# Kernel optimization log

Measured on AMD Instinct MI355X. Metric: run time of the kernel, lower is better.

The kernel has to match this reference:

```python
import jax, jax.numpy as jnp
import numpy as np

# ---- st-moe constants (training-mode routing) ----
EPS = 1e-9
TOP_N = 2
CAP_FACTOR = 1.25      # capacity_factor_train
THRESHOLD = 0.2        # threshold_train (2nd expert)
BAL_COEF = 0.01
Z_COEF = 0.001
MIN_CAP = 4
LN_EPS = 1e-5

B, N, D, E = 4, 2048, 512, 8
H = int(D * 4 * 2 / 3)  # 1365, st-moe default Expert hidden


def _rms_norm(x, gamma):
    # F.normalize(x, dim=-1) * sqrt(d) * gamma
    nrm = jnp.maximum(jnp.linalg.norm(x, axis=-1, keepdims=True), 1e-12)
    return x / nrm * (x.shape[-1] ** 0.5) * gamma


def setup_inputs() -> dict:
    key = jax.random.key(0)
    ks = jax.random.split(key, 6)
    s = 0.02
    return {
        "x": jax.random.normal(ks[0], (B, N, D), jnp.float32),
        "gate_w": jax.random.normal(ks[1], (D, E), jnp.float32) * s,
        "prenorm_g": jnp.ones((D,), jnp.float32),
        "w1": jax.random.normal(ks[2], (E, D, 2 * H), jnp.float32) * s,
        "b1": jnp.zeros((E, 2 * H), jnp.float32),
        "mult_bias": jnp.ones((E, H), jnp.float32),
        "w2": jax.random.normal(ks[3], (E, H, D), jnp.float32) * s,
        "b2": jnp.zeros((E, D), jnp.float32),
        "ln_g": jnp.ones((D,), jnp.float32),
        "ln_b": jnp.zeros((D,), jnp.float32),
    }


def _stmoe_fnn(x, gate_w, prenorm_g, w1, b1, mult_bias, w2, b2, ln_g, ln_b):
    b, n, d = x.shape
    e = gate_w.shape[1]
    cap = max(MIN_CAP, min(n, int(n * CAP_FACTOR / e)))  # static python int

    # SparseMoEBlock: moe(RMSNorm(x)) + x
    xg = _rms_norm(x, prenorm_g)

    # ---- TopNGating ----
    gate_logits = jnp.einsum('bnd,de->bne', xg, gate_w)
    raw_gates = jax.nn.softmax(gate_logits, axis=-1)
    gates, idx = jax.lax.top_k(raw_gates, TOP_N)          # (b,n,k)
    gates = jnp.moveaxis(gates, -1, 0)                    # (k,b,n)
    idx = jnp.moveaxis(idx, -1, 0)                        # (k,b,n)
    one_hot = jax.nn.one_hot(idx, e, dtype=x.dtype)       # (k,b,n,e)

    denom = jnp.maximum(gates.sum(axis=0), EPS)
    gates = gates / denom                                 # normalized top-n scores

    # stochastic routing to non-first experts: prob = min(1, gate/threshold)
    thresh = jnp.array([EPS, THRESHOLD], x.dtype)[:, None, None]
    probs = jax.random.uniform(jax.random.key(42), gates.shape, x.dtype)
    should_route = probs < (gates / jnp.maximum(thresh, EPS))
    should_route = should_route.at[0].set(True)
    mask = one_hot * should_route[..., None].astype(x.dtype)  # (k,b,n,e)

    # exclusive cumsum over sequence -> position within each expert
    mask_cumsum = jnp.cumsum(mask, axis=-2) - mask

    positions, kept_masks = [], []
    prev_count = jnp.zeros((b, 1, e), x.dtype)
    for k in range(TOP_N):  # top_n=2, tiny static loop
        pos_in_expert = (mask_cumsum[k] + prev_count) * mask[k]      # (b,n,e)
        kept = mask[k] * (pos_in_expert < float(cap)).astype(x.dtype)
        prev_count = prev_count + kept.sum(axis=-2, keepdims=True)
        positions.append(pos_in_expert.sum(axis=-1))                 # (b,n)
        kept_masks.append(kept)
    mask = jnp.stack(kept_masks)       # (k,b,n,e) post-capacity
    positions = jnp.stack(positions)   # (k,b,n)

    mask_flat = mask.sum(axis=-1)      # (k,b,n)
    gates = gates * mask_flat

    # safe one-hot: out-of-range (overflow) positions map to all-zeros
    pos_one_hot = jax.nn.one_hot(positions.astype(jnp.int32), cap, dtype=x.dtype)  # (k,b,n,c)
    combine = jnp.einsum('kbn,kbne,kbnc->bnec', gates, one_hot, pos_one_hot)       # (b,n,e,c)

    # straight-through dispatch tensor
    dispatch = (combine > 0).astype(x.dtype) + combine - jax.lax.stop_gradient(combine)

    # ---- dispatch, expert GEGLU FFN, combine ----
    expert_in = jnp.einsum('bnd,bnec->becd', xg, dispatch)                 # (b,e,c,d)
    h = jnp.einsum('becd,edf->becf', expert_in, w1) + b1[None, :, None, :]
    u, g = jnp.split(h, 2, axis=-1)
    act = u * jax.nn.gelu(g, approximate=False) * mult_bias[None, :, None, :]
    expert_out = jnp.einsum('bech,ehd->becd', act, w2) + b2[None, :, None, :]
    moe_out = jnp.einsum('becd,bnec->bnd', expert_out, combine)

    # ---- aux losses (training mode) ----
    density_1 = mask[0].mean(axis=-2)          # (b,e), post-capacity mask (torch in-place view)
    density_proxy = raw_gates.mean(axis=-2)    # (b,e)
    balance_loss = (density_proxy * density_1).mean() * float(e ** 2)
    z = jax.nn.logsumexp(gate_logits, axis=-1)
    router_z_loss = jnp.mean(z * z)
    total_aux = BAL_COEF * balance_loss + Z_COEF * router_z_loss

    # residual, (dropout -> identity for determinism), LayerNorm
    y = moe_out + x
    mu = y.mean(axis=-1, keepdims=True)
    var = jnp.mean((y - mu) ** 2, axis=-1, keepdims=True)
    out = (y - mu) * jax.lax.rsqrt(var + LN_EPS) * ln_g + ln_b
    return out, total_aux


def reference(x, gate_w, prenorm_g, w1, b1, mult_bias, w2, b2, ln_g, ln_b):
    return _stmoe_fnn(x, gate_w, prenorm_g, w1, b1, mult_bias, w2, b2, ln_g, ln_b)
```

## Files before the change

### kernel.cpp

```cpp
#include <hip/hip_runtime.h>
#include <hip/hip_bf16.h>
#include <math.h>

#define BB 4
#define NN 2048
#define DD 512
#define EE 8
#define HH 1365
#define H2 2730
#define CAP 320
#define NT (BB*NN)
#define KP2 1408
#define NW1 2816
#define ME 1280

typedef __bf16 bf16_t;
typedef __bf16 bf16x8 __attribute__((ext_vector_type(8)));
typedef float f32x4 __attribute__((ext_vector_type(4)));

__device__ __forceinline__ float gelu_exact(float x){
    return 0.5f * x * (1.0f + erff(x * 0.70710678118654752f));
}
__device__ __forceinline__ void gl2lds16(const void* g, void* s){
    __builtin_amdgcn_global_load_lds((const __attribute__((address_space(1))) unsigned int*)g,
                                     (__attribute__((address_space(3))) unsigned int*)s,
                                     16, 0, 0);
}
__device__ __forceinline__ unsigned rotl32(unsigned x, int d){ return (x<<d)|(x>>(32-d)); }
__device__ __forceinline__ void tf_round(unsigned &x0, unsigned &x1, int r){
    x0 += x1; x1 = rotl32(x1, r); x1 ^= x0;
}
__device__ float threefry_u01_second(unsigned t){
    const unsigned ks0 = 0u, ks1 = 42u, ks2 = 0x1BD11BDAu ^ 42u;
    unsigned x0 = t, x1 = t + 8192u;
    x0 += ks0; x1 += ks1;
    tf_round(x0,x1,13); tf_round(x0,x1,15); tf_round(x0,x1,26); tf_round(x0,x1,6);
    x0 += ks1; x1 += ks2 + 1u;
    tf_round(x0,x1,17); tf_round(x0,x1,29); tf_round(x0,x1,16); tf_round(x0,x1,24);
    x0 += ks2; x1 += ks0 + 2u;
    tf_round(x0,x1,13); tf_round(x0,x1,15); tf_round(x0,x1,26); tf_round(x0,x1,6);
    x0 += ks0; x1 += ks1 + 3u;
    tf_round(x0,x1,17); tf_round(x0,x1,29); tf_round(x0,x1,16); tf_round(x0,x1,24);
    x0 += ks1; x1 += ks2 + 4u;
    tf_round(x0,x1,13); tf_round(x0,x1,15); tf_round(x0,x1,26); tf_round(x0,x1,6);
    x0 += ks2; x1 += ks0 + 5u;
    unsigned bits = (x1 >> 9) | 0x3f800000u;
    return __uint_as_float(bits) - 1.0f;
}

__global__ void k_gate(const float* __restrict__ x, const float* __restrict__ png,
                       const float* __restrict__ gw, bf16_t* __restrict__ xgb,
                       int* __restrict__ tok_e0, int* __restrict__ tok_e1,
                       float* __restrict__ tok_g0, float* __restrict__ tok_g1,
                       int* __restrict__ tok_c0, int* __restrict__ tok_c1,
                       float* __restrict__ dpPart, float* __restrict__ z2Part){
    if (blockIdx.x == NN){
        xgb[(size_t)NT*DD + threadIdx.x]       = (bf16_t)0.f;
        xgb[(size_t)NT*DD + threadIdx.x + 256] = (bf16_t)0.f;
        return;
    }
    int wave = threadIdx.x >> 6;
    int lane = threadIdx.x & 63;
    int t = blockIdx.x*4 + wave;
    const float* row = x + (size_t)t*DD;
    float xv[8]; float ss = 0.f;
    #pragma unroll
    for (int i=0;i<8;i++){ xv[i] = row[lane + i*64]; ss += xv[i]*xv[i]; }
    #pragma unroll
    for (int off=32; off; off>>=1) ss += __shfl_xor(ss, off);
    float scale = 22.62741699796952f / fmaxf(sqrtf(ss), 1e-12f);
    float acc[EE];
    #pragma unroll
    for (int e=0;e<EE;e++) acc[e]=0.f;
    #pragma unroll
    for (int i=0;i<8;i++){
        int k = lane + i*64;
        float v = xv[i] * scale * png[k];
        xgb[(size_t)t*DD + k] = (bf16_t)v;
        const float* w = gw + k*EE;
        #pragma unroll
        for (int e=0;e<EE;e++) acc[e] = fmaf(v, w[e], acc[e]);
    }
    #pragma unroll
    for (int off=32; off; off>>=1){
        #pragma unroll
        for (int e=0;e<EE;e++) acc[e] += __shfl_down(acc[e], off);
    }
    __shared__ float s_raw[4][EE];
    __shared__ float s_z2[4];
    if (lane==0){
        float mx = acc[0];
        #pragma unroll
        for (int e=1;e<EE;e++) mx = fmaxf(mx, acc[e]);
        float p[EE]; float se=0.f;
        #pragma unroll
        for (int e=0;e<EE;e++){ p[e] = expf(acc[e]-mx); se += p[e]; }
        float inv = 1.f/se;
        #pragma unroll
        for (int e=0;e<EE;e++) p[e] *= inv;
        float z = mx + logf(se);
        int i0=0;
        #pragma unroll
        for (int e=1;e<EE;e++) if (p[e] > p[i0]) i0=e;
        int i1 = (i0==0)?1:0;
        #pragma unroll
        for (int e=0;e<EE;e++){ if (e==i0) continue; if (p[e] > p[i1]) i1=e; }
        float g0=p[i0], g1=p[i1];
        float denom = fmaxf(g0+g1, 1e-9f);
        g0/=denom; g1/=denom;
        float prob = threefry_u01_second((unsigned)t);
        bool route1 = prob < (g1 * 5.0f);
        tok_e0[t] = i0;
        tok_e1[t] = route1 ? i1 : -1;
        tok_g0[t] = g0;
        tok_g1[t] = g1;
        tok_c0[t] = -1;
        tok_c1[t] = -1;
        #pragma unroll
        for (int e=0;e<EE;e++) s_raw[wave][e] = p[e];
        s_z2[wave] = z*z;
    }
    __syncthreads();
    if (threadIdx.x < EE){
        float sum = s_raw[0][threadIdx.x]+s_raw[1][threadIdx.x]+s_raw[2][threadIdx.x]+s_raw[3][threadIdx.x];
        dpPart[threadIdx.x*(size_t)NN + blockIdx.x] = sum;
    }
    if (threadIdx.x == EE) z2Part[blockIdx.x] = s_z2[0]+s_z2[1]+s_z2[2]+s_z2[3];
}

__global__ void k_scan(const int* __restrict__ tok_e0, const int* __restrict__ tok_e1,
                       int* __restrict__ tok_c0, int* __restrict__ tok_c1,
                       int* __restrict__ slot_tok, int* __restrict__ kept0cnt){
    int be = blockIdx.x;
    int b = be >> 3, e = be & 7;
    int tid = threadIdx.x;
    int sbase = (e*BB + b)*CAP;
    for (int i=tid; i<CAP; i+=256) slot_tok[sbase + i] = -1;
    __syncthreads();
    int n0 = tid * 8;
    int base_t = b*NN;
    int m0=0, m1=0;
    for (int i=0;i<8;i++){
        int t = base_t + n0 + i;
        m0 += (tok_e0[t]==e);
        m1 += (tok_e1[t]==e);
    }
    __shared__ int s[256];
    s[tid] = m0 | (m1<<16);
    __syncthreads();
    for (int off=1; off<256; off<<=1){
        int v = 0;
        if (tid >= off) v = s[tid-off];
        __syncthreads();
        if (tid >= off) s[tid] += v;
        __syncthreads();
    }
    int incl = s[tid];
    int total = s[255];
    int p0 = (incl & 0xffff) - m0;
    int p1 = (incl >> 16) - m1;
    int t0 = total & 0xffff;
    int kept0 = min(t0, CAP);
    int c0 = p0, c1 = p1;
    for (int i=0;i<8;i++){
        int n = n0 + i;
        int t = base_t + n;
        if (tok_e0[t]==e){
            int pos = c0++;
            if (pos < CAP){ tok_c0[t] = pos; slot_tok[sbase + pos] = t; }
        }
        if (tok_e1[t]==e){
            int pos = kept0 + c1++;
            if (pos < CAP){ tok_c1[t] = pos; slot_tok[sbase + pos] = t; }
        }
    }
    if (tid==0) kept0cnt[be] = kept0;
}

__global__ void k_aux(const float* __restrict__ dpPart, const float* __restrict__ z2Part,
                      const int* __restrict__ kept0cnt, float* __restrict__ out_aux){
    __shared__ float sdp[32][9];
    __shared__ float sz[256];
    int tid = threadIdx.x;
    float za = 0.f;
    for (int i=tid; i<NN; i+=256) za += z2Part[i];
    sz[tid] = za; __syncthreads();
    for (int off=128; off; off>>=1){ if (tid<off) sz[tid]+=sz[tid+off]; __syncthreads(); }
    int seg = tid >> 3, off8 = tid & 7;
    int b = seg >> 3, e = seg & 7;
    float a = 0.f;
    for (int j=off8; j<512; j+=8) a += dpPart[e*(size_t)NN + b*512 + j];
    sdp[seg][off8] = a;
    __syncthreads();
    if (tid == 0){
        float z2t = sz[0];
        float bal = 0.f;
        for (int sgi=0; sgi<32; sgi++){
            float d = 0.f;
            #pragma unroll
            for (int k=0;k<8;k++) d += sdp[sgi][k];
            float d1 = (float)kept0cnt[sgi] / (float)NN;
            bal += (d / (float)NN) * d1;
        }
        bal = bal / 32.f * 64.f;
        out_aux[0] = 0.01f * bal + 0.001f * (z2t / (float)NT);
    }
}

__global__ void k_w1t(const float* __restrict__ w1, bf16_t* __restrict__ w1t){
    __shared__ float T[32][33];
    int n0 = blockIdx.x * 32;
    int k0 = blockIdx.y * 32;
    int e  = blockIdx.z;
    int tx = threadIdx.x & 31;
    int tg = threadIdx.x >> 5;
    bool half = (n0 >= KP2);
    int nlim = half ? (KP2 + HH) : HH;
    int hoff = half ? (HH - KP2) : 0;
    #pragma unroll
    for (int i=0;i<4;i++){
        int kk = tg + i*8;
        int n = n0 + tx;
        float v = 0.f;
        if (n < nlim) v = w1[((size_t)e*DD + k0 + kk)*H2 + n + hoff];
        T[kk][tx] = v;
    }
    __syncthreads();
    #pragma unroll
    for (int i=0;i<4;i++){
        int nn = tg + i*8;
        w1t[((size_t)e*NW1 + n0 + nn)*DD + k0 + tx] = (bf16_t)T[tx][nn];
    }
}

__global__ void k_w2t(const float* __restrict__ w2, bf16_t* __restrict__ w2t){
    __shared__ float T[32][33];
    int k0 = blockIdx.x * 32;
    int n0 = blockIdx.y * 32;
    int e  = blockIdx.z;
    int tx = threadIdx.x & 31;
    int tg = threadIdx.x >> 5;
    #pragma unroll
    for (int i=0;i<4;i++){
        int kk = tg + i*8;
        float v = 0.f;
        if (k0 + kk < HH) v = w2[((size_t)e*HH + k0 + kk)*DD + n0 + tx];
        T[kk][tx] = v;
    }
    __syncthreads();
    #pragma unroll
    for (int i=0;i<4;i++){
        int nn = tg + i*8;
        w2t[((size_t)e*DD + n0 + nn)*KP2 + k0 + tx] = (bf16_t)T[tx][nn];
    }
}

__global__ __launch_bounds__(256) void k_ffn1_mfma(
    const bf16_t* __restrict__ xgb, const bf16_t* __restrict__ w1t,
    const float* __restrict__ b1, const float* __restrict__ mb,
    const int* __restrict__ slot_tok, bf16_t* __restrict__ actb)
{
    int bid = blockIdx.x;
    int e = bid & 7;
    int r = bid >> 3;
    int m_blk = r % 10, n_blk = r / 10;
    int lane = threadIdx.x & 63, wave = threadIdx.x >> 6;
    int quad = lane >> 4, col = lane & 15;

    __shared__ __align__(16) bf16_t sA[8*512];
    __shared__ __align__(16) bf16_t sBu[4*512];
    __shared__ __align__(16) bf16_t sBg[4*512];

    const bf16_t* gptr[4];
    bf16_t* sptr[4];
    #pragma unroll
    for (int i=0;i<4;i++){
        int id = wave + i*4;
        if (id < 8){
            int slot = slot_tok[e*ME + m_blk*128 + id*16 + col];
            int row = (slot >= 0) ? slot : NT;
            gptr[i] = xgb + (size_t)row*DD + quad*8;
            sptr[i] = sA + id*512;
        } else if (id < 12){
            int n = n_blk*64 + (id-8)*16 + col;
            gptr[i] = w1t + ((size_t)e*NW1 + n)*DD + quad*8;
            sptr[i] = sBu + (id-8)*512;
        } else {
            int n = n_blk*64 + (id-12)*16 + col;
            gptr[i] = w1t + ((size_t)e*NW1 + KP2 + n)*DD + quad*8;
            sptr[i] = sBg + (id-12)*512;
        }
    }

    f32x4 accU[2][4], accG[2][4];
    #pragma unroll
    for (int mi=0;mi<2;mi++)
        #pragma unroll
        for (int ni=0;ni<4;ni++){
            accU[mi][ni] = (f32x4){0.f,0.f,0.f,0.f};
            accG[mi][ni] = (f32x4){0.f,0.f,0.f,0.f};
        }

    for (int ks=0; ks<DD/32; ks++){
        #pragma unroll
        for (int i=0;i<4;i++){ gl2lds16(gptr[i], sptr[i]); gptr[i] += 32; }
        __syncthreads();
        bf16x8 a[2], bu[4], bg[4];
        #pragma unroll
        for (int mi=0;mi<2;mi++) a[mi] = *(const bf16x8*)(sA + (wave*2+mi)*512 + lane*8);
        #pragma unroll
        for (int ni=0;ni<4;ni++){
            bu[ni] = *(const bf16x8*)(sBu + ni*512 + lane*8);
            bg[ni] = *(const bf16x8*)(sBg + ni*512 + lane*8);
        }
        #pragma unroll
        for (int mi=0;mi<2;mi++)
            #pragma unroll
            for (int ni=0;ni<4;ni++){
                accU[mi][ni] = __builtin_amdgcn_mfma_f32_16x16x32_bf16(a[mi], bu[ni], accU[mi][ni], 0,0,0);
                accG[mi][ni] = __builtin_amdgcn_mfma_f32_16x16x32_bf16(a[mi], bg[ni], accG[mi][ni], 0,0,0);
            }
        __syncthreads();
    }
    #pragma unroll
    for (int ni=0; ni<4; ni++){
        int h = n_blk*64 + ni*16 + col;
        bool valid = (h < HH);
        float bu_ = valid ? b1[e*H2 + h] : 0.f;
        float bg_ = valid ? b1[e*H2 + HH + h] : 0.f;
        float mb_ = valid ? mb[e*HH + h] : 0.f;
        #pragma unroll
        for (int mi=0; mi<2; mi++){
            int mrow = m_blk*128 + wave*32 + mi*16 + quad*4;
            #pragma unroll
            for (int rr=0; rr<4; rr++){
                float v = 0.f;
                if (valid){
                    float u = accU[mi][ni][rr] + bu_;
                    float g = accG[mi][ni][rr] + bg_;
                    v = u * gelu_exact(g) * mb_;
                }
                actb[((size_t)e*ME + mrow + rr)*KP2 + h] = (bf16_t)v;
            }
        }
    }
}

__global__ __launch_bounds__(256) void k_ffn2_mfma(
    const bf16_t* __restrict__ actb, const bf16_t* __restrict__ w2t,
    const float* __restrict__ b2, float* __restrict__ eo)
{
    int bid = blockIdx.x;
    int e = bid & 7;
    int r = bid >> 3;
    int m_blk = r % 10, n_blk = r / 10;
    int lane = threadIdx.x & 63, wave = threadIdx.x >> 6;
    int quad = lane >> 4, col = lane & 15;

    __shared__ __align__(16) bf16_t sA[8*512];
    __shared__ __align__(16) bf16_t sB[4*512];

    const bf16_t* gptr[3];
    bf16_t* sptr[3];
    #pragma unroll
    for (int i=0;i<3;i++){
        int id = wave + i*4;
        if (id < 8){
            int mrow = e*ME + m_blk*128 + id*16 + col;
            gptr[i] = actb + (size_t)mrow*KP2 + quad*8;
            sptr[i] = sA + id*512;
        } else {
            int n = n_blk*64 + (id-8)*16 + col;
            gptr[i] = w2t + ((size_t)e*DD + n)*KP2 + quad*8;
            sptr[i] = sB + (id-8)*512;
        }
    }

    f32x4 acc[2][4];
    #pragma unroll
    for (int mi=0;mi<2;mi++)
        #pragma unroll
        for (int ni=0;ni<4;ni++) acc[mi][ni] = (f32x4){0.f,0.f,0.f,0.f};

    for (int ks=0; ks<KP2/32; ks++){
        #pragma unroll
        for (int i=0;i<3;i++){ gl2lds16(gptr[i], sptr[i]); gptr[i] += 32; }
        __syncthreads();
        bf16x8 a[2], bv[4];
        #pragma unroll
        for (int mi=0;mi<2;mi++) a[mi] = *(const bf16x8*)(sA + (wave*2+mi)*512 + lane*8);
        #pragma unroll
        for (int ni=0;ni<4;ni++) bv[ni] = *(const bf16x8*)(sB + ni*512 + lane*8);
        #pragma unroll
        for (int mi=0;mi<2;mi++)
            #pragma unroll
            for (int ni=0;ni<4;ni++)
                acc[mi][ni] = __builtin_amdgcn_mfma_f32_16x16x32_bf16(a[mi], bv[ni], acc[mi][ni], 0,0,0);
        __syncthreads();
    }
    #pragma unroll
    for (int ni=0; ni<4; ni++){
        int d = n_blk*64 + ni*16 + col;
        float bb = b2[e*DD + d];
        #pragma unroll
        for (int mi=0; mi<2; mi++){
            int mrow = m_blk*128 + wave*32 + mi*16 + quad*4;
            #pragma unroll
            for (int rr=0; rr<4; rr++)
                eo[((size_t)e*ME + mrow + rr)*DD + d] = acc[mi][ni][rr] + bb;
        }
    }
}

__global__ void k_combine(const float* __restrict__ x, const float* __restrict__ eo,
        const int* __restrict__ tok_e0, const int* __restrict__ tok_e1,
        const int* __restrict__ tok_c0, const int* __restrict__ tok_c1,
        const float* __restrict__ tok_g0, const float* __restrict__ tok_g1,
        const float* __restrict__ ln_g, const float* __restrict__ ln_b,
        float* __restrict__ out){
    int t = blockIdx.x;
    int b = t / NN;
    int e0 = tok_e0[t], c0 = tok_c0[t];
    int e1 = tok_e1[t], c1 = tok_c1[t];
    float g0 = tok_g0[t], g1 = tok_g1[t];
    const float* r0 = (c0>=0) ? eo + ((size_t)(e0*ME + b*CAP + c0))*DD : nullptr;
    const float* r1 = (e1>=0 && c1>=0) ? eo + ((size_t)(e1*ME + b*CAP + c1))*DD : nullptr;
    float y[2]; float s=0.f, s2=0.f;
    #pragma unroll
    for (int i=0;i<2;i++){
        int d = threadIdx.x + i*256;
        float v = x[(size_t)t*DD + d];
        if (r0) v = fmaf(g0, r0[d], v);
        if (r1) v = fmaf(g1, r1[d], v);
        y[i]=v; s+=v; s2+=v*v;
    }
    __shared__ float rs[4], rs2[4];
    #pragma unroll
    for (int off=32; off; off>>=1){ s+=__shfl_down(s,off); s2+=__shfl_down(s2,off); }
    if ((threadIdx.x&63)==0){ rs[threadIdx.x>>6]=s; rs2[threadIdx.x>>6]=s2; }
    __syncthreads();
    float mu  = (rs[0]+rs[1]+rs[2]+rs[3]) * (1.0f/512.0f);
    float var = (rs2[0]+rs2[1]+rs2[2]+rs2[3]) * (1.0f/512.0f) - mu*mu;
    float inv = rsqrtf(var + 1e-5f);
    #pragma unroll
    for (int i=0;i<2;i++){
        int d = threadIdx.x + i*256;
        out[(size_t)t*DD + d] = (y[i]-mu)*inv*ln_g[d] + ln_b[d];
    }
}

extern "C" void kernel_launch(void* const* d_in, const int* in_sizes, int n_in,
                              void* d_out, int out_size, void* d_ws, size_t ws_size,
                              hipStream_t stream) {
    const float* x         = (const float*)d_in[0];
    const float* gate_w    = (const float*)d_in[1];
    const float* prenorm_g = (const float*)d_in[2];
    const float* w1        = (const float*)d_in[3];
    const float* b1        = (const float*)d_in[4];
    const float* mult_bias = (const float*)d_in[5];
    const float* w2        = (const float*)d_in[6];
    const float* b2        = (const float*)d_in[7];
    const float* ln_g      = (const float*)d_in[8];
    const float* ln_b      = (const float*)d_in[9];
    float* out = (float*)d_out;

    char* p = (char*)d_ws;
    bf16_t* xgb = (bf16_t*)p; p += (size_t)(NT+1)*DD*2;
    bf16_t* w1t = (bf16_t*)p; p += (size_t)EE*NW1*DD*2;
    bf16_t* w2t = (bf16_t*)p; p += (size_t)EE*DD*KP2*2;
    bf16_t* actb = (bf16_t*)p; p += (size_t)EE*ME*KP2*2;
    float* eo  = (float*)p; p += (size_t)EE*ME*DD*4;
    int* slot_tok = (int*)p; p += EE*BB*CAP*4;
    int* tok_e0 = (int*)p; p += NT*4;
    int* tok_e1 = (int*)p; p += NT*4;
    int* tok_c0 = (int*)p; p += NT*4;
    int* tok_c1 = (int*)p; p += NT*4;
    float* tok_g0 = (float*)p; p += NT*4;
    float* tok_g1 = (float*)p; p += NT*4;
    float* dpPart = (float*)p; p += EE*NN*4;
    float* z2Part = (float*)p; p += NN*4;
    int* kept0 = (int*)p; p += BB*EE*4;

    k_w1t<<<dim3(NW1/32, DD/32, EE), 256, 0, stream>>>(w1, w1t);
    k_w2t<<<dim3(KP2/32, DD/32, EE), 256, 0, stream>>>(w2, w2t);
    k_gate<<<NN+1, 256, 0, stream>>>(x, prenorm_g, gate_w, xgb,
                                     tok_e0, tok_e1, tok_g0, tok_g1,
                                     tok_c0, tok_c1, dpPart, z2Part);
    k_scan<<<BB*EE, 256, 0, stream>>>(tok_e0, tok_e1, tok_c0, tok_c1, slot_tok, kept0);
    k_aux<<<1, 256, 0, stream>>>(dpPart, z2Part, kept0, out + (size_t)NT*DD);
    k_ffn1_mfma<<<EE*10*22, 256, 0, stream>>>(xgb, w1t, b1, mult_bias, slot_tok, actb);
    k_ffn2_mfma<<<EE*10*8, 256, 0, stream>>>(actb, w2t, b2, eo);
    k_combine<<<NT, 256, 0, stream>>>(x, eo, tok_e0, tok_e1, tok_c0, tok_c1,
                                      tok_g0, tok_g1, ln_g, ln_b, out);
}
```

Measured before the change: 309.9 us.

## Enlarge MFMA tiles to 128x128 and store weights/activations in K-blocked layout

Both expert GEMMs move from 128x64 output tiles to 128x128 tiles with a 2x2 wave grid, so each wave computes 4x4 MFMA blocks and re-reads less A/B data per output. Transposed weights and the intermediate activations are stored in a K-slice-major layout of 32-wide blocks, so each k-step loads a contiguous chunk. The transpose kernels also write 4-wide bf16 vectors. In exchange, register pressure rises (launch bounds raised to 2 and 4 blocks per CU) and the grids shrink to 880 and 320 blocks, which lowers occupancy and parallelism.

Result: faster. 272.6 us (-12.1%).

```diff
diff --git a/kernel.cpp b/kernel.cpp
--- a/kernel.cpp
+++ b/kernel.cpp
@@ -13,8 +13,11 @@
 #define KP2 1408
 #define NW1 2816
 #define ME 1280
+#define KS1 16
+#define KS2 44
 
 typedef __bf16 bf16_t;
+typedef __bf16 bf16x4 __attribute__((ext_vector_type(4)));
 typedef __bf16 bf16x8 __attribute__((ext_vector_type(8)));
 typedef float f32x4 __attribute__((ext_vector_type(4)));
 
@@ -210,111 +213,119 @@
 __global__ void k_w1t(const float* __restrict__ w1, bf16_t* __restrict__ w1t){
     __shared__ float T[32][33];
     int n0 = blockIdx.x * 32;
-    int k0 = blockIdx.y * 32;
+    int ks = blockIdx.y;
     int e  = blockIdx.z;
     int tx = threadIdx.x & 31;
     int tg = threadIdx.x >> 5;
-    bool half = (n0 >= KP2);
-    int nlim = half ? (KP2 + HH) : HH;
-    int hoff = half ? (HH - KP2) : 0;
+    int n = n0 + tx;
     #pragma unroll
     for (int i=0;i<4;i++){
         int kk = tg + i*8;
-        int n = n0 + tx;
+        int k = ks*32 + kk;
         float v = 0.f;
-        if (n < nlim) v = w1[((size_t)e*DD + k0 + kk)*H2 + n + hoff];
+        if (n < KP2){ if (n < HH) v = w1[((size_t)e*DD + k)*H2 + n]; }
+        else { int h = n - KP2; if (h < HH) v = w1[((size_t)e*DD + k)*H2 + HH + h]; }
         T[kk][tx] = v;
     }
     __syncthreads();
-    #pragma unroll
-    for (int i=0;i<4;i++){
-        int nn = tg + i*8;
-        w1t[((size_t)e*NW1 + n0 + nn)*DD + k0 + tx] = (bf16_t)T[tx][nn];
-    }
+    int rr = threadIdx.x >> 3, s = threadIdx.x & 7;
+    bf16x4 o;
+    #pragma unroll
+    for (int j=0;j<4;j++) o[j] = (bf16_t)T[s*4+j][rr];
+    size_t off = (((size_t)e*KS1 + ks)*NW1 + n0 + rr)*32 + s*4;
+    *(bf16x4*)(w1t + off) = o;
 }
 
 __global__ void k_w2t(const float* __restrict__ w2, bf16_t* __restrict__ w2t){
     __shared__ float T[32][33];
-    int k0 = blockIdx.x * 32;
-    int n0 = blockIdx.y * 32;
+    int n0 = blockIdx.x * 32;
+    int ks = blockIdx.y;
     int e  = blockIdx.z;
     int tx = threadIdx.x & 31;
     int tg = threadIdx.x >> 5;
     #pragma unroll
     for (int i=0;i<4;i++){
         int kk = tg + i*8;
+        int k = ks*32 + kk;
         float v = 0.f;
-        if (k0 + kk < HH) v = w2[((size_t)e*HH + k0 + kk)*DD + n0 + tx];
+        if (k < HH) v = w2[((size_t)e*HH + k)*DD + n0 + tx];
         T[kk][tx] = v;
     }
     __syncthreads();
-    #pragma unroll
-    for (int i=0;i<4;i++){
-        int nn = tg + i*8;
-        w2t[((size_t)e*DD + n0 + nn)*KP2 + k0 + tx] = (bf16_t)T[tx][nn];
-    }
-}
-
-__global__ __launch_bounds__(256) void k_ffn1_mfma(
+    int rr = threadIdx.x >> 3, s = threadIdx.x & 7;
+    bf16x4 o;
+    #pragma unroll
+    for (int j=0;j<4;j++) o[j] = (bf16_t)T[s*4+j][rr];
+    size_t off = (((size_t)e*KS2 + ks)*DD + n0 + rr)*32 + s*4;
+    *(bf16x4*)(w2t + off) = o;
+}
+
+__global__ __launch_bounds__(256,2) void k_ffn1_mfma(
     const bf16_t* __restrict__ xgb, const bf16_t* __restrict__ w1t,
-    const float* __restrict__ b1, const float* __restrict__ mb,
+    const float* __restrict__ b1, const float* __restrict__ mbias,
     const int* __restrict__ slot_tok, bf16_t* __restrict__ actb)
 {
     int bid = blockIdx.x;
     int e = bid & 7;
     int r = bid >> 3;
-    int m_blk = r % 10, n_blk = r / 10;
+    int mblk = r % 10, hb = r / 10;
     int lane = threadIdx.x & 63, wave = threadIdx.x >> 6;
     int quad = lane >> 4, col = lane & 15;
+    int wx = wave & 1, wy = wave >> 1;
 
     __shared__ __align__(16) bf16_t sA[8*512];
-    __shared__ __align__(16) bf16_t sBu[4*512];
-    __shared__ __align__(16) bf16_t sBg[4*512];
-
-    const bf16_t* gptr[4];
-    bf16_t* sptr[4];
-    #pragma unroll
-    for (int i=0;i<4;i++){
-        int id = wave + i*4;
+    __shared__ __align__(16) bf16_t sB[16*512];
+
+    const bf16_t* gsrc[6];
+    bf16_t* sdst[6];
+    int gstep[6];
+    const size_t w1t_e = (size_t)e*KS1*NW1*32;
+    #pragma unroll
+    for (int i=0;i<6;i++){
+        int id = wave + 4*i;
         if (id < 8){
-            int slot = slot_tok[e*ME + m_blk*128 + id*16 + col];
+            int m = mblk*128 + id*16 + col;
+            int slot = slot_tok[e*ME + m];
             int row = (slot >= 0) ? slot : NT;
-            gptr[i] = xgb + (size_t)row*DD + quad*8;
-            sptr[i] = sA + id*512;
-        } else if (id < 12){
-            int n = n_blk*64 + (id-8)*16 + col;
-            gptr[i] = w1t + ((size_t)e*NW1 + n)*DD + quad*8;
-            sptr[i] = sBu + (id-8)*512;
+            gsrc[i] = xgb + (size_t)row*DD + quad*8;
+            sdst[i] = sA + id*512;
+            gstep[i] = 32;
+        } else if (id < 16){
+            int n = hb*128 + (id-8)*16 + col;
+            gsrc[i] = w1t + w1t_e + (size_t)n*32 + quad*8;
+            sdst[i] = sB + (id-8)*512;
+            gstep[i] = NW1*32;
         } else {
-            int n = n_blk*64 + (id-12)*16 + col;
-            gptr[i] = w1t + ((size_t)e*NW1 + KP2 + n)*DD + quad*8;
-            sptr[i] = sBg + (id-12)*512;
-        }
-    }
-
-    f32x4 accU[2][4], accG[2][4];
-    #pragma unroll
-    for (int mi=0;mi<2;mi++)
+            int n = KP2 + hb*128 + (id-16)*16 + col;
+            gsrc[i] = w1t + w1t_e + (size_t)n*32 + quad*8;
+            sdst[i] = sB + (id-8)*512;
+            gstep[i] = NW1*32;
+        }
+    }
+
+    f32x4 accU[4][4], accG[4][4];
+    #pragma unroll
+    for (int mi=0;mi<4;mi++)
         #pragma unroll
         for (int ni=0;ni<4;ni++){
             accU[mi][ni] = (f32x4){0.f,0.f,0.f,0.f};
             accG[mi][ni] = (f32x4){0.f,0.f,0.f,0.f};
         }
 
-    for (int ks=0; ks<DD/32; ks++){
-        #pragma unroll
-        for (int i=0;i<4;i++){ gl2lds16(gptr[i], sptr[i]); gptr[i] += 32; }
+    for (int ks=0; ks<KS1; ks++){
+        #pragma unroll
+        for (int i=0;i<6;i++){ gl2lds16(gsrc[i], sdst[i]); gsrc[i] += gstep[i]; }
         __syncthreads();
-        bf16x8 a[2], bu[4], bg[4];
-        #pragma unroll
-        for (int mi=0;mi<2;mi++) a[mi] = *(const bf16x8*)(sA + (wave*2+mi)*512 + lane*8);
+        bf16x8 a[4], bu[4], bg[4];
+        #pragma unroll
+        for (int mi=0;mi<4;mi++) a[mi] = *(const bf16x8*)(sA + (wx*4+mi)*512 + lane*8);
         #pragma unroll
         for (int ni=0;ni<4;ni++){
-            bu[ni] = *(const bf16x8*)(sBu + ni*512 + lane*8);
-            bg[ni] = *(const bf16x8*)(sBg + ni*512 + lane*8);
-        }
-        #pragma unroll
-        for (int mi=0;mi<2;mi++)
+            bu[ni] = *(const bf16x8*)(sB + (wy*4+ni)*512 + lane*8);
+            bg[ni] = *(const bf16x8*)(sB + (8+wy*4+ni)*512 + lane*8);
+        }
+        #pragma unroll
+        for (int mi=0;mi<4;mi++)
             #pragma unroll
             for (int ni=0;ni<4;ni++){
                 accU[mi][ni] = __builtin_amdgcn_mfma_f32_16x16x32_bf16(a[mi], bu[ni], accU[mi][ni], 0,0,0);
@@ -322,16 +333,20 @@
             }
         __syncthreads();
     }
+
+    const size_t actb_e = (size_t)e*KS2*ME*32;
     #pragma unroll
     for (int ni=0; ni<4; ni++){
-        int h = n_blk*64 + ni*16 + col;
+        int h = hb*128 + wy*64 + ni*16 + col;
         bool valid = (h < HH);
         float bu_ = valid ? b1[e*H2 + h] : 0.f;
         float bg_ = valid ? b1[e*H2 + HH + h] : 0.f;
-        float mb_ = valid ? mb[e*HH + h] : 0.f;
-        #pragma unroll
-        for (int mi=0; mi<2; mi++){
-            int mrow = m_blk*128 + wave*32 + mi*16 + quad*4;
+        float mb_ = valid ? mbias[e*HH + h] : 0.f;
+        int ks2 = h >> 5, kl = h & 31;
+        #pragma unroll
+        for (int mi=0; mi<4; mi++){
+            int m = mblk*128 + wx*64 + mi*16 + quad*4;
+            bf16_t* base = actb + actb_e + ((size_t)ks2*ME + m)*32 + kl;
             #pragma unroll
             for (int rr=0; rr<4; rr++){
                 float v = 0.f;
@@ -340,74 +355,81 @@
                     float g = accG[mi][ni][rr] + bg_;
                     v = u * gelu_exact(g) * mb_;
                 }
-                actb[((size_t)e*ME + mrow + rr)*KP2 + h] = (bf16_t)v;
+                base[rr*32] = (bf16_t)v;
             }
         }
     }
 }
 
-__global__ __launch_bounds__(256) void k_ffn2_mfma(
+__global__ __launch_bounds__(256,4) void k_ffn2_mfma(
     const bf16_t* __restrict__ actb, const bf16_t* __restrict__ w2t,
     const float* __restrict__ b2, float* __restrict__ eo)
 {
     int bid = blockIdx.x;
     int e = bid & 7;
     int r = bid >> 3;
-    int m_blk = r % 10, n_blk = r / 10;
+    int mblk = r % 10, db = r / 10;
     int lane = threadIdx.x & 63, wave = threadIdx.x >> 6;
     int quad = lane >> 4, col = lane & 15;
+    int wx = wave & 1, wy = wave >> 1;
 
     __shared__ __align__(16) bf16_t sA[8*512];
-    __shared__ __align__(16) bf16_t sB[4*512];
-
-    const bf16_t* gptr[3];
-    bf16_t* sptr[3];
-    #pragma unroll
-    for (int i=0;i<3;i++){
-        int id = wave + i*4;
+    __shared__ __align__(16) bf16_t sB[8*512];
+
+    const bf16_t* gsrc[4];
+    bf16_t* sdst[4];
+    int gstep[4];
+    const size_t actb_e = (size_t)e*KS2*ME*32;
+    const size_t w2t_e  = (size_t)e*KS2*DD*32;
+    #pragma unroll
+    for (int i=0;i<4;i++){
+        int id = wave + 4*i;
         if (id < 8){
-            int mrow = e*ME + m_blk*128 + id*16 + col;
-            gptr[i] = actb + (size_t)mrow*KP2 + quad*8;
-            sptr[i] = sA + id*512;
+            int m = mblk*128 + id*16 + col;
+            gsrc[i] = actb + actb_e + (size_t)m*32 + quad*8;
+            sdst[i] = sA + id*512;
+            gstep[i] = ME*32;
         } else {
-            int n = n_blk*64 + (id-8)*16 + col;
-            gptr[i] = w2t + ((size_t)e*DD + n)*KP2 + quad*8;
-            sptr[i] = sB + (id-8)*512;
-        }
-    }
-
-    f32x4 acc[2][4];
-    #pragma unroll
-    for (int mi=0;mi<2;mi++)
+            int d = db*128 + (id-8)*16 + col;
+            gsrc[i] = w2t + w2t_e + (size_t)d*32 + quad*8;
+            sdst[i] = sB + (id-8)*512;
+            gstep[i] = DD*32;
+        }
+    }
+
+    f32x4 acc[4][4];
+    #pragma unroll
+    for (int mi=0;mi<4;mi++)
         #pragma unroll
         for (int ni=0;ni<4;ni++) acc[mi][ni] = (f32x4){0.f,0.f,0.f,0.f};
 
-    for (int ks=0; ks<KP2/32; ks++){
-        #pragma unroll
-        for (int i=0;i<3;i++){ gl2lds16(gptr[i], sptr[i]); gptr[i] += 32; }
+    for (int ks=0; ks<KS2; ks++){
+        #pragma unroll
+        for (int i=0;i<4;i++){ gl2lds16(gsrc[i], sdst[i]); gsrc[i] += gstep[i]; }
         __syncthreads();
-        bf16x8 a[2], bv[4];
-        #pragma unroll
-        for (int mi=0;mi<2;mi++) a[mi] = *(const bf16x8*)(sA + (wave*2+mi)*512 + lane*8);
-        #pragma unroll
-        for (int ni=0;ni<4;ni++) bv[ni] = *(const bf16x8*)(sB + ni*512 + lane*8);
-        #pragma unroll
-        for (int mi=0;mi<2;mi++)
+        bf16x8 a[4], bv[4];
+        #pragma unroll
+        for (int mi=0;mi<4;mi++) a[mi] = *(const bf16x8*)(sA + (wx*4+mi)*512 + lane*8);
+        #pragma unroll
+        for (int ni=0;ni<4;ni++) bv[ni] = *(const bf16x8*)(sB + (wy*4+ni)*512 + lane*8);
+        #pragma unroll
+        for (int mi=0;mi<4;mi++)
             #pragma unroll
             for (int ni=0;ni<4;ni++)
                 acc[mi][ni] = __builtin_amdgcn_mfma_f32_16x16x32_bf16(a[mi], bv[ni], acc[mi][ni], 0,0,0);
         __syncthreads();
     }
+
     #pragma unroll
     for (int ni=0; ni<4; ni++){
-        int d = n_blk*64 + ni*16 + col;
+        int d = db*128 + wy*64 + ni*16 + col;
         float bb = b2[e*DD + d];
         #pragma unroll
-        for (int mi=0; mi<2; mi++){
-            int mrow = m_blk*128 + wave*32 + mi*16 + quad*4;
+        for (int mi=0; mi<4; mi++){
+            int m = mblk*128 + wx*64 + mi*16 + quad*4;
             #pragma unroll
             for (int rr=0; rr<4; rr++)
-                eo[((size_t)e*ME + mrow + rr)*DD + d] = acc[mi][ni][rr] + bb;
+                eo[((size_t)e*ME + m + rr)*DD + d] = acc[mi][ni][rr] + bb;
         }
     }
 }
@@ -466,9 +488,9 @@
 
     char* p = (char*)d_ws;
     bf16_t* xgb = (bf16_t*)p; p += (size_t)(NT+1)*DD*2;
-    bf16_t* w1t = (bf16_t*)p; p += (size_t)EE*NW1*DD*2;
-    bf16_t* w2t = (bf16_t*)p; p += (size_t)EE*DD*KP2*2;
-    bf16_t* actb = (bf16_t*)p; p += (size_t)EE*ME*KP2*2;
+    bf16_t* w1t = (bf16_t*)p; p += (size_t)EE*KS1*NW1*32*2;
+    bf16_t* w2t = (bf16_t*)p; p += (size_t)EE*KS2*DD*32*2;
+    bf16_t* actb = (bf16_t*)p; p += (size_t)EE*KS2*ME*32*2;
     float* eo  = (float*)p; p += (size_t)EE*ME*DD*4;
     int* slot_tok = (int*)p; p += EE*BB*CAP*4;
     int* tok_e0 = (int*)p; p += NT*4;
@@ -481,15 +503,15 @@
     float* z2Part = (float*)p; p += NN*4;
     int* kept0 = (int*)p; p += BB*EE*4;
 
-    k_w1t<<<dim3(NW1/32, DD/32, EE), 256, 0, stream>>>(w1, w1t);
-    k_w2t<<<dim3(KP2/32, DD/32, EE), 256, 0, stream>>>(w2, w2t);
+    k_w1t<<<dim3(NW1/32, KS1, EE), 256, 0, stream>>>(w1, w1t);
+    k_w2t<<<dim3(DD/32, KS2, EE), 256, 0, stream>>>(w2, w2t);
     k_gate<<<NN+1, 256, 0, stream>>>(x, prenorm_g, gate_w, xgb,
                                      tok_e0, tok_e1, tok_g0, tok_g1,
                                      tok_c0, tok_c1, dpPart, z2Part);
     k_scan<<<BB*EE, 256, 0, stream>>>(tok_e0, tok_e1, tok_c0, tok_c1, slot_tok, kept0);
     k_aux<<<1, 256, 0, stream>>>(dpPart, z2Part, kept0, out + (size_t)NT*DD);
-    k_ffn1_mfma<<<EE*10*22, 256, 0, stream>>>(xgb, w1t, b1, mult_bias, slot_tok, actb);
-    k_ffn2_mfma<<<EE*10*8, 256, 0, stream>>>(actb, w2t, b2, eo);
+    k_ffn1_mfma<<<EE*10*11, 256, 0, stream>>>(xgb, w1t, b1, mult_bias, slot_tok, actb);
+    k_ffn2_mfma<<<EE*10*4, 256, 0, stream>>>(actb, w2t, b2, eo);
     k_combine<<<NT, 256, 0, stream>>>(x, eo, tok_e0, tok_e1, tok_c0, tok_c1,
                                       tok_g0, tok_g1, ln_g, ln_b, out);
 }
```
